# Kernel tuning notes

Measured on AMD Instinct MI355X. Metric: run time of the kernel, lower is better.

## Reference

```python
import jax, jax.numpy as jnp
import numpy as np

B, D, C = 4096, 768, 80
PRIV = np.arange(0, 20)        # privileged label indices
NONPRIV = np.arange(20, 80)    # non-privileged label indices
EPS = 1e-8
BETA = 1.0
EPSILON = 0.1
DIMS = [768, 256, 64, 16, 4, 1]


def setup_inputs() -> dict:
    key = jax.random.key(0)
    ks = jax.random.split(key, 12)
    inp = {
        "hidden": jax.random.normal(ks[0], (B, D), dtype=jnp.float32),
        "labels": jax.random.randint(ks[1], (B, C), 0, 2, dtype=jnp.int32),
    }
    ki = 2
    for wpref, bpref in (("W", "b"), ("rW", "rb")):
        for i in range(5):
            din, dout = DIMS[i], DIMS[i + 1]
            inp[f"{wpref}{i+1}"] = (jax.random.normal(ks[ki], (C, din, dout), dtype=jnp.float32)
                                     * (1.0 / np.sqrt(din)))
            inp[f"{bpref}{i+1}"] = jnp.zeros((C, dout), dtype=jnp.float32)
            ki += 1
    return inp


def _scores(hidden, Ws, bs):
    # c independent MLP heads applied to the same hidden state, batched over c.
    x = jnp.einsum('bd,cdh->bch', hidden, Ws[0]) + bs[0]  # (b, c, 256)
    for W, b in zip(Ws[1:], bs[1:]):
        x = jnp.einsum('bch,cho->bco', jax.nn.relu(x), W) + b
    return jax.nn.sigmoid(x[..., 0])  # (b, c)


def _bce(p, y):
    p = jnp.clip(p, EPS, 1.0 - EPS)
    return -(y * jnp.log(p) + (1.0 - y) * jnp.log1p(-p))


def _losses(scores, ref_scores, labels):
    ref_scores = jax.lax.stop_gradient(ref_scores)  # ref head is frozen
    # --- privileged pairwise margin loss (vectorized masked form) ---
    log_term = jnp.log(scores / (ref_scores + EPS) + EPS)  # (b, c)
    ps = scores[:, PRIV]                                   # (b, P)
    pos = labels[:, PRIV] == 1                             # (b, P)
    neg = labels == 0                                      # (b, c)
    # confusing negative k for positive privileged l: y_k==0 and s_k >= s_l
    conf = pos[:, :, None] & neg[:, None, :] & (scores[:, None, :] >= ps[:, :, None])
    h_w = log_term[:, PRIV][:, :, None] - log_term[:, None, :]   # (b, P, c)
    pair_loss = -jax.nn.log_sigmoid(BETA * h_w)
    n_pairs = conf.sum()
    total = jnp.where(conf, pair_loss, 0.0).sum()
    loss_priv = jnp.where(n_pairs > 0, total / jnp.maximum(n_pairs, 1), 0.0)
    # --- non-privileged hinged BCE ---
    y = labels[:, NONPRIV].astype(jnp.float32)
    loss_cur = _bce(scores[:, NONPRIV], y)
    loss_ref = jax.lax.stop_gradient(_bce(ref_scores[:, NONPRIV], y))
    loss_nonpriv = jnp.mean(jax.nn.relu(loss_cur - loss_ref - EPSILON))
    return jnp.stack([loss_priv, loss_nonpriv])


def reference(hidden, labels, W1, b1, W2, b2, W3, b3, W4, b4, W5, b5,
              rW1, rb1, rW2, rb2, rW3, rb3, rW4, rb4, rW5, rb5):
    scores = _scores(hidden, (W1, W2, W3, W4, W5), (b1, b2, b3, b4, b5))
    ref_scores = _scores(hidden, (rW1, rW2, rW3, rW4, rW5), (rb1, rb2, rb3, rb4, rb5))
    return _losses(scores, ref_scores, labels)
```

## Files before the change

kernel.cpp:

```cpp
#include <hip/hip_runtime.h>
#include <math.h>

typedef __attribute__((ext_vector_type(8))) short short8;
typedef __attribute__((ext_vector_type(4))) float f32x4;

#define Bn   4096
#define Dn   768
#define Cn   80
#define H1   256
#define H2   64
#define H3   16
#define H4   4

__device__ inline ushort f2bf(float f) {
    union { float f; unsigned u; } v; v.f = f;
    unsigned r = v.u + 0x7fffu + ((v.u >> 16) & 1u);
    return (ushort)(r >> 16);
}
__device__ inline unsigned pack2(float a, float b) {
    return (unsigned)f2bf(a) | ((unsigned)f2bf(b) << 16);
}
__device__ inline void load_lds16(const void* g, void* l) {
    __builtin_amdgcn_global_load_lds(
        (const __attribute__((address_space(1))) void*)g,
        (__attribute__((address_space(3))) void*)l, 16, 0, 0);
}

#define FENCE() asm volatile("" ::: "memory")
#define BAR() do { FENCE(); __builtin_amdgcn_sched_barrier(0); \
                   __builtin_amdgcn_s_barrier(); \
                   __builtin_amdgcn_sched_barrier(0); FENCE(); } while (0)
#define VMCNT6() do { asm volatile("s_waitcnt vmcnt(6)" ::: "memory"); \
                      __builtin_amdgcn_sched_barrier(0); } while (0)
#define VMCNT0() do { asm volatile("s_waitcnt vmcnt(0)" ::: "memory"); \
                      __builtin_amdgcn_sched_barrier(0); } while (0)

__global__ __launch_bounds__(256)
void convert_hidden(const float* __restrict__ hidden, ushort* __restrict__ hbs)
{
    const int t = threadIdx.x;
    const int kt = blockIdx.x;
    const int bt = blockIdx.y;
    char* out = (char*)hbs + ((size_t)bt * 24 + kt) * 8192;
    #pragma unroll
    for (int ch = 0; ch < 2; ++ch) {
        const int o = (ch * 256 + t) * 16;
        const int r = o >> 6;
        const int s = (o >> 4) & 3;
        const int k0 = (s ^ ((r >> 1) & 3)) * 8;
        const float* src = hidden + (size_t)(bt * 128 + r) * Dn + kt * 32 + k0;
        const float4 f0 = ((const float4*)src)[0];
        const float4 f1 = ((const float4*)src)[1];
        uint4 w;
        w.x = pack2(f0.x, f0.y); w.y = pack2(f0.z, f0.w);
        w.z = pack2(f1.x, f1.y); w.w = pack2(f1.z, f1.w);
        *(uint4*)(out + o) = w;
    }
}

__global__ __launch_bounds__(256)
void convert_w1(const float* __restrict__ W, const float* __restrict__ rW,
                ushort* __restrict__ dst)
{
    __shared__ float l[32 * H1];
    const int t   = threadIdx.x;
    const int kt2 = blockIdx.x;
    const int c   = blockIdx.y;
    const int set = blockIdx.z;
    const float* src = (set ? rW : W) + ((size_t)c * Dn + kt2 * 32) * H1;
    #pragma unroll
    for (int i = 0; i < 8; ++i)
        ((float4*)l)[i * 256 + t] = ((const float4*)src)[i * 256 + t];
    __syncthreads();
    char* out = (char*)dst + (((size_t)set * Cn + c) * 24 + kt2) * 16384;
    #pragma unroll
    for (int rd = 0; rd < 4; ++rd) {
        const int o = (rd * 256 + t) * 16;
        const int n = o >> 6;
        const int s = (o >> 4) & 3;
        const int kk0 = (s ^ ((n >> 1) & 3)) * 8;
        uint4 w;
        w.x = pack2(l[(kk0 + 0) * H1 + n], l[(kk0 + 1) * H1 + n]);
        w.y = pack2(l[(kk0 + 2) * H1 + n], l[(kk0 + 3) * H1 + n]);
        w.z = pack2(l[(kk0 + 4) * H1 + n], l[(kk0 + 5) * H1 + n]);
        w.w = pack2(l[(kk0 + 6) * H1 + n], l[(kk0 + 7) * H1 + n]);
        *(uint4*)(out + o) = w;
    }
}

__global__ __launch_bounds__(256)
void convert_w23(const float* __restrict__ W2, const float* __restrict__ rW2,
                 const float* __restrict__ W3, const float* __restrict__ rW3,
                 ushort* __restrict__ dstW2, ushort* __restrict__ dstW3)
{
    __shared__ float l[64 * H2];
    const int t   = threadIdx.x;
    const int bx  = blockIdx.x;
    const int c   = blockIdx.y;
    const int set = blockIdx.z;

    if (bx < 4) {
        const float* src = (set ? rW2 : W2) + ((size_t)c * H1 + bx * 64) * H2;
        #pragma unroll
        for (int i = 0; i < 4; ++i)
            ((float4*)l)[i * 256 + t] = ((const float4*)src)[i * 256 + t];
        __syncthreads();
        char* out = (char*)dstW2 + (((size_t)set * Cn + c) * 4 + bx) * 8192;
        #pragma unroll
        for (int rd = 0; rd < 2; ++rd) {
            const int idx = rd * 256 + t;
            const int n = idx >> 3;
            const int s = idx & 7;
            const int o = n * 128 + ((s << 4) ^ ((n & 7) << 4));
            const int kk0 = s * 8;
            uint4 w;
            w.x = pack2(l[(kk0 + 0) * H2 + n], l[(kk0 + 1) * H2 + n]);
            w.y = pack2(l[(kk0 + 2) * H2 + n], l[(kk0 + 3) * H2 + n]);
            w.z = pack2(l[(kk0 + 4) * H2 + n], l[(kk0 + 5) * H2 + n]);
            w.w = pack2(l[(kk0 + 6) * H2 + n], l[(kk0 + 7) * H2 + n]);
            *(uint4*)(out + o) = w;
        }
    } else if (t < 128) {
        const float* src = (set ? rW3 : W3) + (size_t)c * (H2 * H3);
        char* out = (char*)dstW3 + ((size_t)set * Cn + c) * 2048;
        const int o = t * 16;
        const int n = o >> 7;
        const int slot = (o >> 4) & 7;
        const int kk0 = (slot ^ (n & 7)) * 8;
        uint4 w;
        w.x = pack2(src[(kk0 + 0) * H3 + n], src[(kk0 + 1) * H3 + n]);
        w.y = pack2(src[(kk0 + 2) * H3 + n], src[(kk0 + 3) * H3 + n]);
        w.z = pack2(src[(kk0 + 4) * H3 + n], src[(kk0 + 5) * H3 + n]);
        w.w = pack2(src[(kk0 + 6) * H3 + n], src[(kk0 + 7) * H3 + n]);
        *(uint4*)(out + o) = w;
    }
}


__device__ __forceinline__ void stageA(char* lds, const char* hb, int slot, int kt, int t) {
    const char* g = hb + (size_t)kt * 8192 + t * 16;
    char* l = lds + slot * 8192 + t * 16;
    load_lds16(g,        l);
    load_lds16(g + 4096, l + 4096);
}
__device__ __forceinline__ void stageB(char* lds, const char* w1b, int slot, int kt, int t) {
    const char* g = w1b + (size_t)kt * 16384 + t * 16;
    char* l = lds + 24576 + slot * 16384 + t * 16;
    load_lds16(g,         l);
    load_lds16(g + 4096,  l + 4096);
    load_lds16(g + 8192,  l + 8192);
    load_lds16(g + 12288, l + 12288);
}

__global__ __launch_bounds__(256, 2)
void scores_mfma_w128(const ushort* __restrict__ hbs, const ushort* __restrict__ W1ts,
                      const ushort* __restrict__ W2ts, const ushort* __restrict__ W3ts,
                      const float* __restrict__ b1, const float* __restrict__ rb1,
                      const float* __restrict__ b2, const float* __restrict__ rb2,
                      const float* __restrict__ b3, const float* __restrict__ rb3,
                      const float* __restrict__ W4, const float* __restrict__ rW4,
                      const float* __restrict__ b4, const float* __restrict__ rb4,
                      const float* __restrict__ W5, const float* __restrict__ rW5,
                      const float* __restrict__ b5, const float* __restrict__ rb5,
                      float* __restrict__ scores)
{
    __shared__ uint4 smv[73728 / 16];
    char* lds = (char*)smv;

    const int t = threadIdx.x;
    const int wid = t >> 6, lane = t & 63;
    const int lrow = lane & 15;
    const int lkg  = lane >> 4;
    const int lk   = lkg * 8;
    const int wr  = wid >> 1;
    const int wcn = wid & 1;

    const int cpx = 5120 >> 3;
    const int wg  = (blockIdx.x & 7) * cpx + (blockIdx.x >> 3);
    const int set = wg / 2560;
    const int rem = wg % 2560;
    const int c   = rem / 32;
    const int bt  = rem % 32;

    const float* pb1 = set ? rb1 : b1;
    const float* pb2 = set ? rb2 : b2;
    const float* pb3 = set ? rb3 : b3;
    const float* pW4 = set ? rW4 : W4;  const float* pb4 = set ? rb4 : b4;
    const float* pW5 = set ? rW5 : W5;  const float* pb5 = set ? rb5 : b5;

    const char* hb  = (const char*)hbs + (size_t)bt * 196608;
    const char* w1b = (const char*)W1ts + (size_t)(set * Cn + c) * 393216;

    f32x4 acc[4][8];
    #pragma unroll
    for (int i = 0; i < 4; ++i)
        #pragma unroll
        for (int j = 0; j < 8; ++j)
            acc[i][j] = (f32x4){0.f, 0.f, 0.f, 0.f};

    stageA(lds, hb, 0, 0, t);  stageB(lds, w1b, 0, 0, t);
    stageA(lds, hb, 1, 1, t);  stageB(lds, w1b, 1, 1, t);
    VMCNT6();
    BAR();

    #pragma unroll 3
    for (int j = 0; j < 24; ++j) {
        const int rs = j % 3;
        short8 breg[8], areg[4];
        {
            const char* bb = lds + 24576 + rs * 16384;
            const char* ab = lds + rs * 8192;
            #pragma unroll
            for (int nt = 0; nt < 8; ++nt) {
                const int col = wcn * 128 + nt * 16 + lrow;
                breg[nt] = *(const short8*)(bb + col * 64
                              + ((2 * lk) ^ (((col >> 1) & 3) << 4)));
            }
            #pragma unroll
            for (int mt = 0; mt < 4; ++mt) {
                const int row = wr * 64 + mt * 16 + lrow;
                areg[mt] = *(const short8*)(ab + row * 64
                              + ((2 * lk) ^ (((row >> 1) & 3) << 4)));
            }
        }
        {
            const int ws = (j + 2) % 3;
            int ka = j + 2; if (ka >= 24) ka -= 24;
            stageA(lds, hb, ws, ka, t);
            stageB(lds, w1b, ws, ka, t);
        }
        VMCNT6();
        BAR();
        __builtin_amdgcn_s_setprio(1);
        #pragma unroll
        for (int mt = 0; mt < 4; ++mt)
            #pragma unroll
            for (int nt = 0; nt < 8; ++nt)
                acc[mt][nt] = __builtin_amdgcn_mfma_f32_16x16x32_bf16(
                    breg[nt], areg[mt], acc[mt][nt], 0, 0, 0);
        __builtin_amdgcn_s_setprio(0);
        BAR();
    }
    VMCNT0();
    BAR();

    {
        float4 bias1[8];
        #pragma unroll
        for (int nt = 0; nt < 8; ++nt)
            bias1[nt] = *(const float4*)&pb1[(size_t)c * H1 + wcn * 128 + nt * 16 + lkg * 4];
        #pragma unroll
        for (int mt = 0; mt < 4; ++mt) {
            const int row = wr * 64 + mt * 16 + lrow;
            const int swz = (row & 7) << 4;
            #pragma unroll
            for (int nt = 0; nt < 8; ++nt) {
                const float* bb = (const float*)&bias1[nt];
                uint2 w;
                w.x = pack2(fmaxf(acc[mt][nt][0] + bb[0], 0.f),
                            fmaxf(acc[mt][nt][1] + bb[1], 0.f));
                w.y = pack2(fmaxf(acc[mt][nt][2] + bb[2], 0.f),
                            fmaxf(acc[mt][nt][3] + bb[3], 0.f));
                const int off = row * 512 + ((wcn * 256 + nt * 32 + lkg * 8) ^ swz);
                *(uint2*)(lds + off) = w;
            }
        }
    }
    BAR();

    f32x4 acc2[2][4];
    #pragma unroll
    for (int i = 0; i < 2; ++i)
        #pragma unroll
        for (int j = 0; j < 4; ++j)
            acc2[i][j] = (f32x4){0.f, 0.f, 0.f, 0.f};
    {
        const char* w2b = (const char*)W2ts + (size_t)(set * Cn + c) * 32768;
        #pragma unroll
        for (int ksz = 0; ksz < 8; ++ksz) {
            short8 b2r[4], a2[2];
            const int kk2 = (ksz & 1) * 32 + lk;
            #pragma unroll
            for (int nt = 0; nt < 4; ++nt) {
                const int col = nt * 16 + lrow;
                b2r[nt] = *(const short8*)(w2b + (ksz >> 1) * 8192
                             + ((col * 128 + 2 * kk2) ^ ((col & 7) << 4)));
            }
            const int k = ksz * 32 + lk;
            #pragma unroll
            for (int m2 = 0; m2 < 2; ++m2) {
                const int row = wid * 32 + m2 * 16 + lrow;
                a2[m2] = *(const short8*)(lds + ((row * 512 + 2 * k) ^ ((row & 7) << 4)));
            }
            #pragma unroll
            for (int m2 = 0; m2 < 2; ++m2)
                #pragma unroll
                for (int nt = 0; nt < 4; ++nt)
                    acc2[m2][nt] = __builtin_amdgcn_mfma_f32_16x16x32_bf16(
                        b2r[nt], a2[m2], acc2[m2][nt], 0, 0, 0);
        }
    }
    BAR();

    {
        float4 bias2[4];
        #pragma unroll
        for (int nt = 0; nt < 4; ++nt)
            bias2[nt] = *(const float4*)&pb2[(size_t)c * H2 + nt * 16 + lkg * 4];
        #pragma unroll
        for (int m2 = 0; m2 < 2; ++m2) {
            const int row = wid * 32 + m2 * 16 + lrow;
            const int swz = (row & 7) << 4;
            #pragma unroll
            for (int nt = 0; nt < 4; ++nt) {
                const float* bb = (const float*)&bias2[nt];
                uint2 w;
                w.x = pack2(fmaxf(acc2[m2][nt][0] + bb[0], 0.f),
                            fmaxf(acc2[m2][nt][1] + bb[1], 0.f));
                w.y = pack2(fmaxf(acc2[m2][nt][2] + bb[2], 0.f),
                            fmaxf(acc2[m2][nt][3] + bb[3], 0.f));
                const int off = row * 128 + ((nt * 32 + lkg * 8) ^ swz);
                *(uint2*)(lds + off) = w;
            }
        }
    }
    BAR();

    {
        const char* w3t = (const char*)W3ts + (size_t)(set * Cn + c) * 2048;
        short8 w3f[2];
        #pragma unroll
        for (int ks = 0; ks < 2; ++ks)
            w3f[ks] = *(const short8*)(w3t + lrow * 128
                         + ((2 * (ks * 32 + lk)) ^ ((lrow & 7) << 4)));
        f32x4 acc3[2];
        #pragma unroll
        for (int m2 = 0; m2 < 2; ++m2) acc3[m2] = (f32x4){0.f, 0.f, 0.f, 0.f};
        #pragma unroll
        for (int m2 = 0; m2 < 2; ++m2) {
            const int row = wid * 32 + m2 * 16 + lrow;
            #pragma unroll
            for (int ks = 0; ks < 2; ++ks) {
                const short8 xf = *(const short8*)(lds + row * 128
                                     + ((2 * (ks * 32 + lk)) ^ ((row & 7) << 4)));
                acc3[m2] = __builtin_amdgcn_mfma_f32_16x16x32_bf16(
                    w3f[ks], xf, acc3[m2], 0, 0, 0);
            }
        }

        const float4 b3v = *(const float4*)&pb3[(size_t)c * H3 + lkg * 4];
        const float* w4c = pW4 + (size_t)c * (H3 * H4);
        float4 w4r[4];
        #pragma unroll
        for (int r = 0; r < 4; ++r)
            w4r[r] = *(const float4*)&w4c[(lkg * 4 + r) * H4];
        const float4 b4v = *(const float4*)&pb4[(size_t)c * H4];
        const float4 w5v = *(const float4*)&pW5[(size_t)c * H4];
        const float bb5 = pb5[c];

        #pragma unroll
        for (int m2 = 0; m2 < 2; ++m2) {
            float p4[4] = {0.f, 0.f, 0.f, 0.f};
            #pragma unroll
            for (int r = 0; r < 4; ++r) {
                const float x3 = fmaxf(acc3[m2][r] + ((const float*)&b3v)[r], 0.f);
                const float* wr4 = (const float*)&w4r[r];
                #pragma unroll
                for (int o = 0; o < 4; ++o)
                    p4[o] = fmaf(x3, wr4[o], p4[o]);
            }
            #pragma unroll
            for (int o = 0; o < 4; ++o) {
                p4[o] += __shfl_xor(p4[o], 16, 64);
                p4[o] += __shfl_xor(p4[o], 32, 64);
            }
            float x5 = bb5;
            #pragma unroll
            for (int o = 0; o < 4; ++o)
                x5 = fmaf(fmaxf(p4[o] + ((const float*)&b4v)[o], 0.f),
                          ((const float*)&w5v)[o], x5);
            const float sc = 1.f / (1.f + expf(-x5));
            if (lkg == 0)
                scores[((size_t)set * Bn + bt * 128 + wid * 32 + m2 * 16 + lrow) * Cn + c] = sc;
        }
    }
}

__device__ inline float bce_f(float p, float y) {
    p = fminf(fmaxf(p, 1e-8f), 1.0f - 1e-8f);
    return -(y * logf(p) + (1.f - y) * log1pf(-p));
}

__global__ __launch_bounds__(128)
void loss_kernel(const float* __restrict__ scores, const int* __restrict__ labels,
                 float* __restrict__ pair_sum, float* __restrict__ np_sum,
                 int* __restrict__ pair_cnt)
{
    __shared__ float ss[Cn], lt[Cn];
    __shared__ int lab[Cn];
    __shared__ float redf[128], redn[128];
    __shared__ int redi[128];

    const int b = blockIdx.x, t = threadIdx.x;
    float np_local = 0.f, ps_local = 0.f;
    int pc_local = 0;

    if (t < Cn) {
        const float s  = scores[(size_t)b * Cn + t];
        const float sr = scores[(size_t)Bn * Cn + (size_t)b * Cn + t];
        const int l = labels[(size_t)b * Cn + t];
        ss[t] = s; lab[t] = l;
        lt[t] = logf(s / (sr + 1e-8f) + 1e-8f);
        if (t >= 20) {
            const float y = (float)l;
            np_local = fmaxf(bce_f(s, y) - bce_f(sr, y) - 0.1f, 0.f);
        }
    }
    __syncthreads();
    if (t < Cn && lab[t] == 0) {
        const float sj = ss[t], ltj = lt[t];
        #pragma unroll
        for (int i = 0; i < 20; ++i) {
            if (lab[i] == 1 && sj >= ss[i]) {
                const float z = -(lt[i] - ltj);
                ps_local += fmaxf(z, 0.f) + log1pf(expf(-fabsf(z)));
                pc_local++;
            }
        }
    }
    redf[t] = ps_local; redn[t] = np_local; redi[t] = pc_local;
    __syncthreads();
    for (int s = 64; s > 0; s >>= 1) {
        if (t < s) { redf[t] += redf[t + s]; redn[t] += redn[t + s]; redi[t] += redi[t + s]; }
        __syncthreads();
    }
    if (t == 0) { pair_sum[b] = redf[0]; np_sum[b] = redn[0]; pair_cnt[b] = redi[0]; }
}

__global__ __launch_bounds__(1024)
void final_kernel(const float* __restrict__ pair_sum, const int* __restrict__ pair_cnt,
                  const float* __restrict__ np_sum, float* __restrict__ out)
{
    __shared__ float r1[1024], r2[1024];
    __shared__ int ri[1024];
    const int t = threadIdx.x;
    float s1 = 0.f, s2 = 0.f; int c1 = 0;
    for (int i = t; i < Bn; i += 1024) { s1 += pair_sum[i]; c1 += pair_cnt[i]; s2 += np_sum[i]; }
    r1[t] = s1; r2[t] = s2; ri[t] = c1;
    __syncthreads();
    for (int s = 512; s > 0; s >>= 1) {
        if (t < s) { r1[t] += r1[t + s]; r2[t] += r2[t + s]; ri[t] += ri[t + s]; }
        __syncthreads();
    }
    if (t == 0) {
        const int n = ri[0];
        out[0] = (n > 0) ? (r1[0] / (float)(n > 1 ? n : 1)) : 0.f;
        out[1] = r2[0] / (float)(Bn * 60);
    }
}

static inline size_t alup(size_t x) { return (x + 4095) & ~(size_t)4095; }

extern "C" void kernel_launch(void* const* d_in, const int* in_sizes, int n_in,
                              void* d_out, int out_size, void* d_ws, size_t ws_size,
                              hipStream_t stream)
{
    const float* hidden = (const float*)d_in[0];
    const int*   labels = (const int*)d_in[1];
    const float* W1 = (const float*)d_in[2];   const float* b1 = (const float*)d_in[3];
    const float* W2 = (const float*)d_in[4];   const float* b2 = (const float*)d_in[5];
    const float* W3 = (const float*)d_in[6];   const float* b3 = (const float*)d_in[7];
    const float* W4 = (const float*)d_in[8];   const float* b4 = (const float*)d_in[9];
    const float* W5 = (const float*)d_in[10];  const float* b5 = (const float*)d_in[11];
    const float* rW1 = (const float*)d_in[12]; const float* rb1 = (const float*)d_in[13];
    const float* rW2 = (const float*)d_in[14]; const float* rb2 = (const float*)d_in[15];
    const float* rW3 = (const float*)d_in[16]; const float* rb3 = (const float*)d_in[17];
    const float* rW4 = (const float*)d_in[18]; const float* rb4 = (const float*)d_in[19];
    const float* rW5 = (const float*)d_in[20]; const float* rb5 = (const float*)d_in[21];

    char* ws = (char*)d_ws;
    const size_t off_scores = 0;
    const size_t sz_scores  = (size_t)2 * Bn * Cn * 4;
    const size_t off_pair   = alup(off_scores + sz_scores);
    const size_t sz_pair    = (size_t)3 * Bn * 4;
    const size_t off_hbs    = alup(off_pair + sz_pair);
    const size_t sz_hbs     = (size_t)Bn * Dn * 2;
    const size_t off_w1t    = alup(off_hbs + sz_hbs);
    const size_t sz_w1t     = (size_t)2 * Cn * 24 * 16384;
    const size_t off_w2t    = alup(off_w1t + sz_w1t);
    const size_t sz_w2t     = (size_t)2 * Cn * 4 * 8192;
    const size_t off_w3t    = alup(off_w2t + sz_w2t);

    float* scoresb  = (float*)(ws + off_scores);
    float* pair_sum = (float*)(ws + off_pair);
    float* np_sum   = pair_sum + Bn;
    int*   pair_cnt = (int*)(np_sum + Bn);
    float* out      = (float*)d_out;

    ushort* hbs  = (ushort*)(ws + off_hbs);
    ushort* W1ts = (ushort*)(ws + off_w1t);
    ushort* W2ts = (ushort*)(ws + off_w2t);
    ushort* W3ts = (ushort*)(ws + off_w3t);

    convert_hidden<<<dim3(24, Bn / 128), 256, 0, stream>>>(hidden, hbs);
    convert_w1<<<dim3(24, Cn, 2), 256, 0, stream>>>(W1, rW1, W1ts);
    convert_w23<<<dim3(5, Cn, 2), 256, 0, stream>>>(W2, rW2, W3, rW3, W2ts, W3ts);

    scores_mfma_w128<<<5120, 256, 0, stream>>>(hbs, W1ts, W2ts, W3ts,
        b1, rb1, b2, rb2, b3, rb3, W4, rW4, b4, rb4, W5, rW5, b5, rb5,
        scoresb);
    loss_kernel<<<Bn, 128, 0, stream>>>(scoresb, labels, pair_sum, np_sum, pair_cnt);
    final_kernel<<<1, 1024, 0, stream>>>(pair_sum, pair_cnt, np_sum, out);
}
```

Measured before the change: 340.1 us.

## Split W1 k-step into four interleaved phases of LDS reads, loads, and MFMAs

Restructures the main GEMM loop so each k-step runs in four phases. Each phase reads two B fragments from LDS, issues part of the next stage's global-to-LDS loads, and runs 8 MFMAs, with barriers and lgkmcnt waits between phases. The goal is to interleave memory traffic with matrix math and cut register pressure from holding all eight B fragments at once. The cost is more barriers per iteration (eight instead of two), which may add synchronisation stalls.

```diff
diff --git a/kernel.cpp b/kernel.cpp
--- a/kernel.cpp
+++ b/kernel.cpp
@@ -30,6 +30,8 @@
 #define BAR() do { FENCE(); __builtin_amdgcn_sched_barrier(0); \
                    __builtin_amdgcn_s_barrier(); \
                    __builtin_amdgcn_sched_barrier(0); FENCE(); } while (0)
+#define LGKM0() do { asm volatile("s_waitcnt lgkmcnt(0)" ::: "memory"); \
+                     __builtin_amdgcn_sched_barrier(0); } while (0)
 #define VMCNT6() do { asm volatile("s_waitcnt vmcnt(6)" ::: "memory"); \
                       __builtin_amdgcn_sched_barrier(0); } while (0)
 #define VMCNT0() do { asm volatile("s_waitcnt vmcnt(0)" ::: "memory"); \
@@ -143,13 +145,12 @@
     load_lds16(g,        l);
     load_lds16(g + 4096, l + 4096);
 }
-__device__ __forceinline__ void stageB(char* lds, const char* w1b, int slot, int kt, int t) {
-    const char* g = w1b + (size_t)kt * 16384 + t * 16;
-    char* l = lds + 24576 + slot * 16384 + t * 16;
-    load_lds16(g,         l);
-    load_lds16(g + 4096,  l + 4096);
-    load_lds16(g + 8192,  l + 8192);
-    load_lds16(g + 12288, l + 12288);
+__device__ __forceinline__ void stageBh(char* lds, const char* w1b, int slot, int kt,
+                                        int half, int t) {
+    const char* g = w1b + (size_t)kt * 16384 + half * 8192 + t * 16;
+    char* l = lds + 24576 + slot * 16384 + half * 8192 + t * 16;
+    load_lds16(g,        l);
+    load_lds16(g + 4096, l + 4096);
 }
 
 __global__ __launch_bounds__(256, 2)
@@ -198,49 +199,70 @@
         for (int j = 0; j < 8; ++j)
             acc[i][j] = (f32x4){0.f, 0.f, 0.f, 0.f};
 
-    stageA(lds, hb, 0, 0, t);  stageB(lds, w1b, 0, 0, t);
-    stageA(lds, hb, 1, 1, t);  stageB(lds, w1b, 1, 1, t);
+    stageA(lds, hb, 0, 0, t);
+    stageBh(lds, w1b, 0, 0, 0, t); stageBh(lds, w1b, 0, 0, 1, t);
+    stageA(lds, hb, 1, 1, t);
+    stageBh(lds, w1b, 1, 1, 0, t); stageBh(lds, w1b, 1, 1, 1, t);
     VMCNT6();
     BAR();
+
+    #define RD_B(dst, NT) do {                                              \
+        const int col_ = wcn * 128 + (NT) * 16 + lrow;                      \
+        dst = *(const short8*)(bb + col_ * 64                               \
+                  + ((2 * lk) ^ (((col_ >> 1) & 3) << 4))); } while (0)
+    #define PH_MFMA(bv0, bv1, N0, N1) do {                                  \
+        __builtin_amdgcn_s_setprio(1);                                      \
+        _Pragma("unroll")                                                   \
+        for (int mt_ = 0; mt_ < 4; ++mt_)                                   \
+            acc[mt_][N0] = __builtin_amdgcn_mfma_f32_16x16x32_bf16(         \
+                bv0, areg[mt_], acc[mt_][N0], 0, 0, 0);                     \
+        _Pragma("unroll")                                                   \
+        for (int mt_ = 0; mt_ < 4; ++mt_)                                   \
+            acc[mt_][N1] = __builtin_amdgcn_mfma_f32_16x16x32_bf16(         \
+                bv1, areg[mt_], acc[mt_][N1], 0, 0, 0);                     \
+        __builtin_amdgcn_s_setprio(0); } while (0)
 
     #pragma unroll 3
     for (int j = 0; j < 24; ++j) {
         const int rs = j % 3;
-        short8 breg[8], areg[4];
-        {
-            const char* bb = lds + 24576 + rs * 16384;
-            const char* ab = lds + rs * 8192;
-            #pragma unroll
-            for (int nt = 0; nt < 8; ++nt) {
-                const int col = wcn * 128 + nt * 16 + lrow;
-                breg[nt] = *(const short8*)(bb + col * 64
-                              + ((2 * lk) ^ (((col >> 1) & 3) << 4)));
-            }
-            #pragma unroll
-            for (int mt = 0; mt < 4; ++mt) {
-                const int row = wr * 64 + mt * 16 + lrow;
-                areg[mt] = *(const short8*)(ab + row * 64
-                              + ((2 * lk) ^ (((row >> 1) & 3) << 4)));
-            }
-        }
-        {
-            const int ws = (j + 2) % 3;
-            int ka = j + 2; if (ka >= 24) ka -= 24;
-            stageA(lds, hb, ws, ka, t);
-            stageB(lds, w1b, ws, ka, t);
-        }
+        const int ws = (j + 2) % 3;
+        int ka = j + 2; if (ka >= 24) ka -= 24;
+        const char* bb = lds + 24576 + rs * 16384;
+        const char* ab = lds + rs * 8192;
+        short8 areg[4], bA, bB;
+
+        #pragma unroll
+        for (int mt = 0; mt < 4; ++mt) {
+            const int row = wr * 64 + mt * 16 + lrow;
+            areg[mt] = *(const short8*)(ab + row * 64
+                          + ((2 * lk) ^ (((row >> 1) & 3) << 4)));
+        }
+        RD_B(bA, 0); RD_B(bB, 1);
+        stageA(lds, hb, ws, ka, t);
+        BAR(); LGKM0();
+        PH_MFMA(bA, bB, 0, 1);
+        BAR();
+
+        RD_B(bA, 2); RD_B(bB, 3);
+        stageBh(lds, w1b, ws, ka, 0, t);
+        BAR(); LGKM0();
+        PH_MFMA(bA, bB, 2, 3);
+        BAR();
+
+        RD_B(bA, 4); RD_B(bB, 5);
+        stageBh(lds, w1b, ws, ka, 1, t);
+        BAR(); LGKM0();
+        PH_MFMA(bA, bB, 4, 5);
+        BAR();
+
+        RD_B(bA, 6); RD_B(bB, 7);
         VMCNT6();
+        BAR(); LGKM0();
+        PH_MFMA(bA, bB, 6, 7);
         BAR();
-        __builtin_amdgcn_s_setprio(1);
-        #pragma unroll
-        for (int mt = 0; mt < 4; ++mt)
-            #pragma unroll
-            for (int nt = 0; nt < 8; ++nt)
-                acc[mt][nt] = __builtin_amdgcn_mfma_f32_16x16x32_bf16(
-                    breg[nt], areg[mt], acc[mt][nt], 0, 0, 0);
-        __builtin_amdgcn_s_setprio(0);
-        BAR();
-    }
+    }
+    #undef RD_B
+    #undef PH_MFMA
     VMCNT0();
     BAR();
 
```

Measured after the change: 338.3 us. About the same (-0.5%).

## Load hidden A-tiles directly from global into registers, bypassing LDS staging

Applied to the files above, without the earlier changes.

The hidden-state A operand is no longer staged through LDS with global_load_lds. Each wave now loads its pre-swizzled A fragments straight from global memory into registers, one k-tile ahead, while only the W1 B operand keeps the triple-buffered LDS pipeline. This cuts LDS footprint and LDS read traffic per iteration, and it adjusts the vmcnt waits to cover the extra in-flight register loads. The cost is more global loads per wave, since each of the two column waves re-reads the same A rows, and more registers for the double-buffered A fragments. Global latency may now be exposed right before the MFMAs.

```diff
diff --git a/kernel.cpp b/kernel.cpp
--- a/kernel.cpp
+++ b/kernel.cpp
@@ -30,9 +30,14 @@
 #define BAR() do { FENCE(); __builtin_amdgcn_sched_barrier(0); \
                    __builtin_amdgcn_s_barrier(); \
                    __builtin_amdgcn_sched_barrier(0); FENCE(); } while (0)
-#define VMCNT6() do { asm volatile("s_waitcnt vmcnt(6)" ::: "memory"); \
+#define VMCNT8() do { __builtin_amdgcn_sched_barrier(0); \
+                      asm volatile("s_waitcnt vmcnt(8)" ::: "memory"); \
                       __builtin_amdgcn_sched_barrier(0); } while (0)
-#define VMCNT0() do { asm volatile("s_waitcnt vmcnt(0)" ::: "memory"); \
+#define VMCNT4() do { __builtin_amdgcn_sched_barrier(0); \
+                      asm volatile("s_waitcnt vmcnt(4)" ::: "memory"); \
+                      __builtin_amdgcn_sched_barrier(0); } while (0)
+#define VMCNT0() do { __builtin_amdgcn_sched_barrier(0); \
+                      asm volatile("s_waitcnt vmcnt(0)" ::: "memory"); \
                       __builtin_amdgcn_sched_barrier(0); } while (0)
 
 __global__ __launch_bounds__(256)
@@ -137,19 +142,24 @@
 }
 
 
-__device__ __forceinline__ void stageA(char* lds, const char* hb, int slot, int kt, int t) {
-    const char* g = hb + (size_t)kt * 8192 + t * 16;
-    char* l = lds + slot * 8192 + t * 16;
-    load_lds16(g,        l);
-    load_lds16(g + 4096, l + 4096);
-}
 __device__ __forceinline__ void stageB(char* lds, const char* w1b, int slot, int kt, int t) {
     const char* g = w1b + (size_t)kt * 16384 + t * 16;
-    char* l = lds + 24576 + slot * 16384 + t * 16;
+    char* l = lds + slot * 16384 + t * 16;
     load_lds16(g,         l);
     load_lds16(g + 4096,  l + 4096);
     load_lds16(g + 8192,  l + 8192);
     load_lds16(g + 12288, l + 12288);
+}
+
+__device__ __forceinline__ void loadA(short8 a[4], const char* hb, int kt,
+                                      int wr, int lrow, int lkg) {
+    const char* tb = hb + (size_t)kt * 8192;
+    #pragma unroll
+    for (int mt = 0; mt < 4; ++mt) {
+        const int row = wr * 64 + mt * 16 + lrow;
+        a[mt] = *(const short8*)(tb + row * 64
+                    + ((lkg * 16) ^ ((((row >> 1) & 3)) << 4)));
+    }
 }
 
 __global__ __launch_bounds__(256, 2)
@@ -164,7 +174,7 @@
                       const float* __restrict__ b5, const float* __restrict__ rb5,
                       float* __restrict__ scores)
 {
-    __shared__ uint4 smv[73728 / 16];
+    __shared__ uint4 smv[65536 / 16];
     char* lds = (char*)smv;
 
     const int t = threadIdx.x;
@@ -198,38 +208,33 @@
         for (int j = 0; j < 8; ++j)
             acc[i][j] = (f32x4){0.f, 0.f, 0.f, 0.f};
 
-    stageA(lds, hb, 0, 0, t);  stageB(lds, w1b, 0, 0, t);
-    stageA(lds, hb, 1, 1, t);  stageB(lds, w1b, 1, 1, t);
-    VMCNT6();
+    short8 aC[4], aN[4];
+    loadA(aC, hb, 0, wr, lrow, lkg);
+    stageB(lds, w1b, 0, 0, t);
+    stageB(lds, w1b, 1, 1, t);
+    VMCNT4();
     BAR();
 
     #pragma unroll 3
     for (int j = 0; j < 24; ++j) {
         const int rs = j % 3;
-        short8 breg[8], areg[4];
+        const int ws = (j + 2) % 3;
+        int ka = j + 2; if (ka >= 24) ka -= 24;
+        int ja = j + 1; if (ja >= 24) ja -= 24;
+
+        loadA(aN, hb, ja, wr, lrow, lkg);
+        short8 breg[8];
         {
-            const char* bb = lds + 24576 + rs * 16384;
-            const char* ab = lds + rs * 8192;
+            const char* bb = lds + rs * 16384;
             #pragma unroll
             for (int nt = 0; nt < 8; ++nt) {
                 const int col = wcn * 128 + nt * 16 + lrow;
                 breg[nt] = *(const short8*)(bb + col * 64
                               + ((2 * lk) ^ (((col >> 1) & 3) << 4)));
             }
-            #pragma unroll
-            for (int mt = 0; mt < 4; ++mt) {
-                const int row = wr * 64 + mt * 16 + lrow;
-                areg[mt] = *(const short8*)(ab + row * 64
-                              + ((2 * lk) ^ (((row >> 1) & 3) << 4)));
-            }
-        }
-        {
-            const int ws = (j + 2) % 3;
-            int ka = j + 2; if (ka >= 24) ka -= 24;
-            stageA(lds, hb, ws, ka, t);
-            stageB(lds, w1b, ws, ka, t);
-        }
-        VMCNT6();
+        }
+        stageB(lds, w1b, ws, ka, t);
+        VMCNT8();
         BAR();
         __builtin_amdgcn_s_setprio(1);
         #pragma unroll
@@ -237,9 +242,11 @@
             #pragma unroll
             for (int nt = 0; nt < 8; ++nt)
                 acc[mt][nt] = __builtin_amdgcn_mfma_f32_16x16x32_bf16(
-                    breg[nt], areg[mt], acc[mt][nt], 0, 0, 0);
+                    breg[nt], aC[mt], acc[mt][nt], 0, 0, 0);
         __builtin_amdgcn_s_setprio(0);
         BAR();
+        #pragma unroll
+        for (int mt = 0; mt < 4; ++mt) aC[mt] = aN[mt];
     }
     VMCNT0();
     BAR();
```

After: 348.8 us. 1.03x slower.
